# Kernel tuning notes

Measured on AMD Instinct MI355X. Metric: run time of the kernel, lower is better.

## Reference

```python
import jax, jax.numpy as jnp
import numpy as np

T_TYPES = 3
IN_DIM = 128
HID = 128
B = 8192
N_ALLY = 15
N_OPP = 16
N_NODES = 1 + N_ALLY + N_OPP


def setup_inputs() -> dict:
    key = jax.random.key(0)
    k1, k2, k3, k4 = jax.random.split(key, 4)
    h = jax.random.normal(k1, (B, N_NODES, IN_DIM), dtype=jnp.float32)
    ALL_TYPE_MASK = jax.random.bernoulli(k2, 0.4, (T_TYPES, B, N_NODES))
    # learned params (xavier-ish scale)
    W = jax.random.normal(k3, (T_TYPES, IN_DIM, HID), dtype=jnp.float32) * 0.1
    a = jax.random.normal(k4, (T_TYPES, 2 * HID, 1), dtype=jnp.float32) * 0.1
    return {"h": h, "ALL_TYPE_MASK": ALL_TYPE_MASK, "num_ally": N_ALLY,
            "num_opp": N_OPP, "self_type": 0, "W": W, "a": a}


def _het_gat(h, ALL_TYPE_MASK, num_ally, num_opp, W, a):
    T, hid = W.shape[0], W.shape[-1]
    mask_self = ALL_TYPE_MASK[:, :, 0]                       # (T,B) True -> this type's W used for self
    mask_ally = ALL_TYPE_MASK[:, :, 1:1 + num_ally]          # (T,B,Na)
    mask_opp = ALL_TYPE_MASK[:, :, 1 + num_ally:]            # (T,B,No)
    h_self = h[:, 0, :]                                      # (B,D)
    h_ally = h[:, 1:1 + num_ally, :]                         # (B,Na,D)
    h_opp = h[:, 1 + num_ally:, :]                           # (B,No,D)
    # per-type projections (the original loops over types; batched einsum here)
    H_SELF = jnp.einsum('bd,tdh->tbh', h_self, W)            # (T,B,H)
    H_ALLY = jnp.einsum('bnd,tdh->tbnh', h_ally, W)          # (T,B,Na,H)
    H_OPP = jnp.einsum('bnd,tdh->tbnh', h_opp, W)            # (T,B,No,H)
    a_top = a[:, :hid, 0]                                    # (T,H) acts on self part
    a_bot = a[:, hid:, 0]                                    # (T,H) acts on neighbor part

    def att_sum(H_nb, mask_nb):
        # score e[b,i,j,n] = [H_SELF[i,b] ; H_nb[j,b,n]] @ a[j]
        # decomposed dot avoids materializing the (T,T,B,N,2H) concat tensor
        s_self = jnp.einsum('ibh,jh->ijb', H_SELF, a_top)    # (T,T,B)
        s_nb = jnp.einsum('jbnh,jh->jbn', H_nb, a_bot)       # (T,B,N)
        e = s_self[:, :, :, None] + s_nb[None, :, :, :]      # (T,T,B,N) axes i,j,b,n
        m = jnp.broadcast_to(mask_nb[None], e.shape)         # mask indexed by (j,b,n), bcast over i
        Bb = e.shape[2]
        e_flat = jnp.transpose(e, (2, 0, 1, 3)).reshape(Bb, -1)   # (B, T*T*N)
        m_flat = jnp.transpose(m, (2, 0, 1, 3)).reshape(Bb, -1)
        neg_inf = jnp.asarray(-jnp.inf, e_flat.dtype)
        attn = jax.nn.softmax(jnp.where(m_flat, neg_inf, e_flat), axis=-1)
        attn = jnp.where(m_flat, jnp.zeros((), attn.dtype), attn)
        attn4 = attn.reshape(Bb, T, T, -1)                   # (B,i,j,n)
        # weighted sum over flattened (i,j,n) of H_nb[j,b,n]
        return jnp.einsum('bijn,jbnh->bh', attn4, H_nb)      # (B,H)

    ally_ws = att_sum(H_ALLY, mask_ally)
    opp_ws = att_sum(H_OPP, mask_opp)
    h_self_sum = jnp.einsum('tbh,tb->bh', H_SELF, mask_self.astype(H_SELF.dtype))
    return jax.nn.elu(h_self_sum + ally_ws + opp_ws)         # (B,H)


def reference(h, ALL_TYPE_MASK, num_ally, num_opp, self_type, W, a):
    return _het_gat(h, ALL_TYPE_MASK, num_ally, num_opp, W, a)
```

## Files before the change

### kernel.cpp

```cpp
#include <hip/hip_runtime.h>
#include <math.h>

#define NB 8192
#define G 4
#define NBLK (NB / G)
#define NNODES 32
#define TT 3
#define DIM 128
#define HID 128
#define HSTR 132

__global__ __launch_bounds__(128) void gat_prep(
    const float* __restrict__ Wg,
    const float* __restrict__ ag,
    float* __restrict__ uv)
{
    int e = blockIdx.x, d = threadIdx.x;
    int wi, aoff;
    if (e < 9) { wi = e / 3; aoff = (e % 3) * 2 * HID; }
    else       { wi = e - 9; aoff = wi * 2 * HID + HID; }
    const float* wrow = Wg + wi * DIM * HID + d * HID;
    const float* arow = ag + aoff;
    float acc = 0.f;
    #pragma unroll 16
    for (int h = 0; h < HID; ++h) acc += wrow[h] * arow[h];
    uv[e * DIM + d] = acc;
}

__global__ __launch_bounds__(256, 4) void gat_main(
    const float* __restrict__ hg,
    const int* __restrict__ maskg,
    const float* __restrict__ Wg,
    const float* __restrict__ uv,
    float* __restrict__ outg)
{
    __shared__ float hL[NNODES * HSTR];
    __shared__ float uvL[12 * HSTR];
    __shared__ float sTop[16];
    __shared__ float sNb[96];
    __shared__ float vv[TT * NNODES];
    __shared__ float gAll[G * TT * DIM];
    __shared__ float pL[4 * G * DIM];
    __shared__ int   mvL[G * 96];

    const int tid = threadIdx.x;
    const int b0 = blockIdx.x * G;

    #pragma unroll
    for (int k = 0; k < 6; ++k) {
        int idx = tid + k * 256;
        uvL[(idx >> 7) * HSTR + (idx & 127)] = uv[idx];
    }
    if (tid < 96) {
        int t = tid >> 5, node = tid & 31;
        #pragma unroll
        for (int g = 0; g < G; ++g)
            mvL[g * 96 + tid] = maskg[(size_t)t * NB * NNODES + (size_t)(b0 + g) * NNODES + node];
    }
    __syncthreads();

    for (int g = 0; g < G; ++g) {
        {
            const float4* src = (const float4*)(hg + (size_t)(b0 + g) * (NNODES * DIM));
            #pragma unroll
            for (int k = 0; k < 4; ++k) {
                int idx = tid + k * 256;
                float4 v = src[idx];
                int f = idx << 2;
                *(float4*)&hL[(f >> 7) * HSTR + (f & 127)] = v;
            }
        }
        __syncthreads();

        if (tid < 210) {
            int task = tid >> 1, half = tid & 1;
            const float4 *hp, *vp;
            if (task < 96) {
                int t = task >> 5, n = task & 31;
                hp = (const float4*)&hL[n * HSTR];
                vp = (const float4*)&uvL[(9 + t) * HSTR];
            } else {
                int e = task - 96;
                hp = (const float4*)&hL[0];
                vp = (const float4*)&uvL[e * HSTR];
            }
            hp += half * 16; vp += half * 16;
            float acc = 0.f;
            #pragma unroll
            for (int q = 0; q < 16; ++q) {
                float4 x = hp[q], y = vp[q];
                acc += x.x * y.x + x.y * y.y + x.z * y.z + x.w * y.w;
            }
            acc += __shfl_xor(acc, 1, 64);
            if (!half) {
                if (task < 96) sNb[task] = acc;
                else           sTop[task - 96] = acc;
            }
        }
        __syncthreads();

        int wv = tid >> 6;
        if (wv == 0) {
            int lane = tid;
            bool act = lane < 45;
            int j = act ? lane / 15 : 0;
            int n = act ? lane % 15 : 0;
            int mk = 1; float sv = 0.f;
            if (act) {
                mk = mvL[g * 96 + j * 32 + 1 + n];
                sv = sNb[j * 32 + 1 + n];
            }
            float e0 = sTop[0 + j] + sv;
            float e1 = sTop[3 + j] + sv;
            float e2 = sTop[6 + j] + sv;
            bool live = act && (mk == 0);
            float lm = live ? fmaxf(e0, fmaxf(e1, e2)) : -__builtin_inff();
            #pragma unroll
            for (int off = 32; off; off >>= 1) lm = fmaxf(lm, __shfl_xor(lm, off, 64));
            float es = live ? (expf(e0 - lm) + expf(e1 - lm) + expf(e2 - lm)) : 0.f;
            float Z = es;
            #pragma unroll
            for (int off = 32; off; off >>= 1) Z += __shfl_xor(Z, off, 64);
            float w = (live && Z > 0.f) ? es / Z : 0.f;
            if (act) vv[j * NNODES + 1 + n] = w;
        } else if (wv == 1) {
            int lane = tid - 64;
            bool act = lane < 48;
            int j = act ? (lane >> 4) : 0;
            int n = act ? (lane & 15) : 0;
            int mk = 1; float sv = 0.f;
            if (act) {
                mk = mvL[g * 96 + j * 32 + 16 + n];
                sv = sNb[j * 32 + 16 + n];
            }
            float e0 = sTop[0 + j] + sv;
            float e1 = sTop[3 + j] + sv;
            float e2 = sTop[6 + j] + sv;
            bool live = act && (mk == 0);
            float lm = live ? fmaxf(e0, fmaxf(e1, e2)) : -__builtin_inff();
            #pragma unroll
            for (int off = 32; off; off >>= 1) lm = fmaxf(lm, __shfl_xor(lm, off, 64));
            float es = live ? (expf(e0 - lm) + expf(e1 - lm) + expf(e2 - lm)) : 0.f;
            float Z = es;
            #pragma unroll
            for (int off = 32; off; off >>= 1) Z += __shfl_xor(Z, off, 64);
            float w = (live && Z > 0.f) ? es / Z : 0.f;
            if (act) vv[j * NNODES + 16 + n] = w;
        } else if (wv == 2) {
            int lane = tid - 128;
            if (lane < 3)
                vv[lane * NNODES + 0] = mvL[g * 96 + lane * 32 + 0] ? 1.f : 0.f;
        }
        __syncthreads();

        if (tid < 128) {
            int d = tid;
            float a0 = 0.f, a1 = 0.f, a2 = 0.f;
            #pragma unroll
            for (int n = 0; n < NNODES; ++n) {
                float hv = hL[n * HSTR + d];
                a0 += vv[n] * hv;
                a1 += vv[NNODES + n] * hv;
                a2 += vv[2 * NNODES + n] * hv;
            }
            float* gp = &gAll[g * TT * DIM];
            gp[d] = a0; gp[DIM + d] = a1; gp[2 * DIM + d] = a2;
        }
        __syncthreads();
    }

    {
        int hp2 = tid & 63;
        int dq  = tid >> 6;
        float2 acc[G];
        #pragma unroll
        for (int g = 0; g < G; ++g) acc[g] = make_float2(0.f, 0.f);
        #pragma unroll
        for (int t = 0; t < TT; ++t) {
            const float* wbase = Wg + ((size_t)t * DIM + dq * 32) * HID;
            const float* gbase = &gAll[t * DIM + dq * 32];
            #pragma unroll 8
            for (int dd = 0; dd < 32; ++dd) {
                float2 wq = *(const float2*)(wbase + dd * HID + 2 * hp2);
                #pragma unroll
                for (int g = 0; g < G; ++g) {
                    float gv = gbase[g * TT * DIM + dd];
                    acc[g].x += gv * wq.x;
                    acc[g].y += gv * wq.y;
                }
            }
        }
        #pragma unroll
        for (int g = 0; g < G; ++g)
            *(float2*)&pL[(dq * G + g) * DIM + 2 * hp2] = acc[g];
    }
    __syncthreads();

    #pragma unroll
    for (int r = 0; r < 2; ++r) {
        int idx = tid + r * 256;
        int g = idx >> 7, h = idx & 127;
        float s = pL[idx] + pL[512 + idx] + pL[1024 + idx] + pL[1536 + idx];
        float rr = (s > 0.f) ? s : expm1f(s);
        outg[(size_t)(b0 + g) * DIM + h] = rr;
    }
}

extern "C" void kernel_launch(void* const* d_in, const int* in_sizes, int n_in,
                              void* d_out, int out_size, void* d_ws, size_t ws_size,
                              hipStream_t stream) {
    const float* hg    = (const float*)d_in[0];
    const int*   maskg = (const int*)d_in[1];
    const float* Wg    = (const float*)d_in[5];
    const float* ag    = (const float*)d_in[6];
    float* uv = (float*)d_ws;
    float* outg = (float*)d_out;

    gat_prep<<<12, 128, 0, stream>>>(Wg, ag, uv);
    gat_main<<<NBLK, 256, 0, stream>>>(hg, maskg, Wg, uv, outg);
}
```

Measured before the change: 231.3 us.

## Double-buffer node features in LDS with swizzle and register-resident score vectors

```diff
diff --git a/kernel.cpp b/kernel.cpp
--- a/kernel.cpp
+++ b/kernel.cpp
@@ -8,7 +8,6 @@
 #define TT 3
 #define DIM 128
 #define HID 128
-#define HSTR 132
 
 __global__ __launch_bounds__(128) void gat_prep(
     const float* __restrict__ Wg,
@@ -27,6 +26,13 @@
     uv[e * DIM + d] = acc;
 }
 
+__device__ __forceinline__ int swz_slot(int n, int c) { return n * 32 + (c ^ (n & 7)); }
+
+__device__ __forceinline__ void lds_barrier() {
+    asm volatile("s_waitcnt lgkmcnt(0)" ::: "memory");
+    __builtin_amdgcn_s_barrier();
+}
+
 __global__ __launch_bounds__(256, 4) void gat_main(
     const float* __restrict__ hg,
     const int* __restrict__ maskg,
@@ -34,70 +40,90 @@
     const float* __restrict__ uv,
     float* __restrict__ outg)
 {
-    __shared__ float hL[NNODES * HSTR];
-    __shared__ float uvL[12 * HSTR];
+    __shared__ __align__(16) float hL[2 * NNODES * DIM];
+    __shared__ float gAll[G * TT * DIM];
     __shared__ float sTop[16];
-    __shared__ float sNb[96];
-    __shared__ float vv[TT * NNODES];
-    __shared__ float gAll[G * TT * DIM];
-    __shared__ float pL[4 * G * DIM];
+    __shared__ float sNb[TT * NNODES];
     __shared__ int   mvL[G * 96];
 
     const int tid = threadIdx.x;
     const int b0 = blockIdx.x * G;
-
+    const int dq = tid & 3;
+
+    int urow;
+    if (tid < 192) urow = 9 + (tid >> 6);
+    else           urow = (tid - 192) >> 2;
+    if (urow > 11) urow = 0;
+    float4 uvreg[8];
     #pragma unroll
-    for (int k = 0; k < 6; ++k) {
-        int idx = tid + k * 256;
-        uvL[(idx >> 7) * HSTR + (idx & 127)] = uv[idx];
-    }
+    for (int k = 0; k < 8; ++k)
+        uvreg[k] = *(const float4*)(uv + urow * DIM + 4 * (dq + 4 * k));
+
     if (tid < 96) {
         int t = tid >> 5, node = tid & 31;
         #pragma unroll
         for (int g = 0; g < G; ++g)
             mvL[g * 96 + tid] = maskg[(size_t)t * NB * NNODES + (size_t)(b0 + g) * NNODES + node];
     }
+
+    {
+        const float4* src = (const float4*)(hg + (size_t)b0 * (NNODES * DIM));
+        float4 p0[4];
+        #pragma unroll
+        for (int k = 0; k < 4; ++k) p0[k] = src[tid + k * 256];
+        #pragma unroll
+        for (int k = 0; k < 4; ++k) {
+            int idx = tid + k * 256;
+            ((float4*)hL)[swz_slot(idx >> 5, idx & 31)] = p0[k];
+        }
+    }
     __syncthreads();
 
+    float4 pre[4];
+
     for (int g = 0; g < G; ++g) {
-        {
-            const float4* src = (const float4*)(hg + (size_t)(b0 + g) * (NNODES * DIM));
-            #pragma unroll
-            for (int k = 0; k < 4; ++k) {
-                int idx = tid + k * 256;
-                float4 v = src[idx];
-                int f = idx << 2;
-                *(float4*)&hL[(f >> 7) * HSTR + (f & 127)] = v;
-            }
-        }
-        __syncthreads();
-
-        if (tid < 210) {
-            int task = tid >> 1, half = tid & 1;
-            const float4 *hp, *vp;
-            if (task < 96) {
-                int t = task >> 5, n = task & 31;
-                hp = (const float4*)&hL[n * HSTR];
-                vp = (const float4*)&uvL[(9 + t) * HSTR];
+        const float* hb = hL + (g & 1) * (NNODES * DIM);
+
+        if (g + 1 < G) {
+            const float4* src = (const float4*)(hg + (size_t)(b0 + g + 1) * (NNODES * DIM));
+            #pragma unroll
+            for (int k = 0; k < 4; ++k) pre[k] = src[tid + k * 256];
+        }
+
+        if (tid < 228) {
+            const float4* hb4 = (const float4*)hb;
+            if (tid < 192) {
+                int task4 = tid >> 2;
+                int t  = task4 >> 4;
+                int n0 = (task4 & 15) * 2;
+                float a0 = 0.f, a1 = 0.f;
+                #pragma unroll
+                for (int k = 0; k < 8; ++k) {
+                    int c = dq + 4 * k;
+                    float4 x0 = hb4[swz_slot(n0,     c)];
+                    float4 x1 = hb4[swz_slot(n0 + 1, c)];
+                    float4 u  = uvreg[k];
+                    a0 += x0.x*u.x + x0.y*u.y + x0.z*u.z + x0.w*u.w;
+                    a1 += x1.x*u.x + x1.y*u.y + x1.z*u.z + x1.w*u.w;
+                }
+                a0 += __shfl_xor(a0, 1, 64); a0 += __shfl_xor(a0, 2, 64);
+                a1 += __shfl_xor(a1, 1, 64); a1 += __shfl_xor(a1, 2, 64);
+                if (dq == 0) { sNb[t * 32 + n0] = a0; sNb[t * 32 + n0 + 1] = a1; }
             } else {
-                int e = task - 96;
-                hp = (const float4*)&hL[0];
-                vp = (const float4*)&uvL[e * HSTR];
-            }
-            hp += half * 16; vp += half * 16;
-            float acc = 0.f;
-            #pragma unroll
-            for (int q = 0; q < 16; ++q) {
-                float4 x = hp[q], y = vp[q];
-                acc += x.x * y.x + x.y * y.y + x.z * y.z + x.w * y.w;
-            }
-            acc += __shfl_xor(acc, 1, 64);
-            if (!half) {
-                if (task < 96) sNb[task] = acc;
-                else           sTop[task - 96] = acc;
-            }
-        }
-        __syncthreads();
+                int e = (tid - 192) >> 2;
+                float a = 0.f;
+                #pragma unroll
+                for (int k = 0; k < 8; ++k) {
+                    int c = dq + 4 * k;
+                    float4 x = hb4[c];
+                    float4 u = uvreg[k];
+                    a += x.x*u.x + x.y*u.y + x.z*u.z + x.w*u.w;
+                }
+                a += __shfl_xor(a, 1, 64); a += __shfl_xor(a, 2, 64);
+                if (dq == 0) sTop[e] = a;
+            }
+        }
+        lds_barrier();
 
         int wv = tid >> 6;
         if (wv == 0) {
@@ -122,7 +148,7 @@
             #pragma unroll
             for (int off = 32; off; off >>= 1) Z += __shfl_xor(Z, off, 64);
             float w = (live && Z > 0.f) ? es / Z : 0.f;
-            if (act) vv[j * NNODES + 1 + n] = w;
+            if (act) sNb[j * 32 + 1 + n] = w;
         } else if (wv == 1) {
             int lane = tid - 64;
             bool act = lane < 48;
@@ -145,54 +171,67 @@
             #pragma unroll
             for (int off = 32; off; off >>= 1) Z += __shfl_xor(Z, off, 64);
             float w = (live && Z > 0.f) ? es / Z : 0.f;
-            if (act) vv[j * NNODES + 16 + n] = w;
+            if (act) sNb[j * 32 + 16 + n] = w;
         } else if (wv == 2) {
             int lane = tid - 128;
             if (lane < 3)
-                vv[lane * NNODES + 0] = mvL[g * 96 + lane * 32 + 0] ? 1.f : 0.f;
-        }
-        __syncthreads();
+                sNb[lane * 32 + 0] = mvL[g * 96 + lane * 32 + 0] ? 1.f : 0.f;
+        }
+        lds_barrier();
 
         if (tid < 128) {
             int d = tid;
+            int chi = d >> 2, clo = d & 3;
             float a0 = 0.f, a1 = 0.f, a2 = 0.f;
             #pragma unroll
             for (int n = 0; n < NNODES; ++n) {
-                float hv = hL[n * HSTR + d];
-                a0 += vv[n] * hv;
-                a1 += vv[NNODES + n] * hv;
-                a2 += vv[2 * NNODES + n] * hv;
+                float hv = hb[n * DIM + ((chi ^ (n & 7)) << 2) + clo];
+                a0 += sNb[n] * hv;
+                a1 += sNb[NNODES + n] * hv;
+                a2 += sNb[2 * NNODES + n] * hv;
             }
             float* gp = &gAll[g * TT * DIM];
             gp[d] = a0; gp[DIM + d] = a1; gp[2 * DIM + d] = a2;
         }
-        __syncthreads();
+
+        if (g + 1 < G) {
+            float* nb = hL + ((g + 1) & 1) * (NNODES * DIM);
+            #pragma unroll
+            for (int k = 0; k < 4; ++k) {
+                int idx = tid + k * 256;
+                ((float4*)nb)[swz_slot(idx >> 5, idx & 31)] = pre[k];
+            }
+        }
+        lds_barrier();
     }
 
     {
-        int hp2 = tid & 63;
-        int dq  = tid >> 6;
-        float2 acc[G];
-        #pragma unroll
-        for (int g = 0; g < G; ++g) acc[g] = make_float2(0.f, 0.f);
+        int hq  = tid & 31;
+        int dq8 = tid >> 5;
+        float4 acc[G];
+        #pragma unroll
+        for (int g = 0; g < G; ++g) acc[g] = make_float4(0.f, 0.f, 0.f, 0.f);
         #pragma unroll
         for (int t = 0; t < TT; ++t) {
-            const float* wbase = Wg + ((size_t)t * DIM + dq * 32) * HID;
-            const float* gbase = &gAll[t * DIM + dq * 32];
-            #pragma unroll 8
-            for (int dd = 0; dd < 32; ++dd) {
-                float2 wq = *(const float2*)(wbase + dd * HID + 2 * hp2);
+            const float* wbase = Wg + ((size_t)t * DIM + dq8 * 16) * HID + 4 * hq;
+            const float* gbase = &gAll[t * DIM + dq8 * 16];
+            #pragma unroll 4
+            for (int dd = 0; dd < 16; ++dd) {
+                float4 wq = *(const float4*)(wbase + dd * HID);
                 #pragma unroll
                 for (int g = 0; g < G; ++g) {
                     float gv = gbase[g * TT * DIM + dd];
                     acc[g].x += gv * wq.x;
                     acc[g].y += gv * wq.y;
+                    acc[g].z += gv * wq.z;
+                    acc[g].w += gv * wq.w;
                 }
             }
         }
+        float* pL = hL;
         #pragma unroll
         for (int g = 0; g < G; ++g)
-            *(float2*)&pL[(dq * G + g) * DIM + 2 * hp2] = acc[g];
+            *(float4*)&pL[(dq8 * G + g) * DIM + 4 * hq] = acc[g];
     }
     __syncthreads();
 
@@ -200,7 +239,9 @@
     for (int r = 0; r < 2; ++r) {
         int idx = tid + r * 256;
         int g = idx >> 7, h = idx & 127;
-        float s = pL[idx] + pL[512 + idx] + pL[1024 + idx] + pL[1536 + idx];
+        float s = 0.f;
+        #pragma unroll
+        for (int p = 0; p < 8; ++p) s += hL[p * 512 + idx];
         float rr = (s > 0.f) ? s : expm1f(s);
         outg[(size_t)(b0 + g) * DIM + h] = rr;
     }
```

Result: slower. 289.1 us (+25.0%).
